# Optimization experiments

Measured on AMD Instinct MI355X. Metric: run time of the kernel, lower is better.

## Reference

```python
import jax, jax.numpy as jnp
import numpy as np

D = 384      # n_embed_dims
H = 6        # n_heads
HS = D // H  # head_size = 64
T = 256      # block_size
B = 256
EPS = 1e-5


def setup_inputs() -> dict:
    key = jax.random.key(0)
    ks = jax.random.split(key, 12)
    s_in = 1.0 / np.sqrt(D)
    s_ff = 1.0 / np.sqrt(4 * D)
    return {
        "x": jax.random.normal(ks[0], (B, T, D), jnp.float32),
        # per-head QKV weights, stacked [H, D, HS] (Linear bias=False)
        "wq": jax.random.normal(ks[1], (H, D, HS), jnp.float32) * s_in,
        "wk": jax.random.normal(ks[2], (H, D, HS), jnp.float32) * s_in,
        "wv": jax.random.normal(ks[3], (H, D, HS), jnp.float32) * s_in,
        "w_proj": jax.random.normal(ks[4], (D, D), jnp.float32) * s_in,
        "b_proj": jax.random.normal(ks[5], (D,), jnp.float32) * s_in,
        "w1": jax.random.normal(ks[6], (D, 4 * D), jnp.float32) * s_in,
        "b1": jax.random.normal(ks[7], (4 * D,), jnp.float32) * s_in,
        "w2": jax.random.normal(ks[8], (4 * D, D), jnp.float32) * s_ff,
        "b2": jax.random.normal(ks[9], (D,), jnp.float32) * s_ff,
        "g1": jnp.ones((D,), jnp.float32),
        "be1": jnp.zeros((D,), jnp.float32),
        "g2": jnp.ones((D,), jnp.float32),
        "be2": jnp.zeros((D,), jnp.float32),
    }


def _layernorm(x, g, b):
    mu = jnp.mean(x, axis=-1, keepdims=True)
    var = jnp.mean(jnp.square(x - mu), axis=-1, keepdims=True)
    return (x - mu) * jax.lax.rsqrt(var + EPS) * g + b


def _attention(x, wq, wk, wv, w_proj, b_proj):
    # faithful quirk: scale = 1/sqrt(C) with C = full embed dim (384)
    scale = 1.0 / jnp.sqrt(jnp.asarray(D, x.dtype))
    q = jnp.einsum("btd,hde->bhte", x, wq)  # [B,H,T,HS]
    k = jnp.einsum("btd,hde->bhte", x, wk)
    v = jnp.einsum("btd,hde->bhte", x, wv)
    w = jnp.einsum("bhte,bhse->bhts", q, k) * scale  # [B,H,T,T], no mask
    w = jax.nn.softmax(w, axis=-1)
    out = jnp.einsum("bhts,bhse->bhte", w, v)  # [B,H,T,HS]
    # concat heads along feature dim (head order matches torch cat)
    out = out.transpose(0, 2, 1, 3).reshape(x.shape[0], x.shape[1], D)
    return out @ w_proj + b_proj


def reference(x, wq, wk, wv, w_proj, b_proj, w1, b1, w2, b2, g1, be1, g2, be2):
    x = x + _attention(_layernorm(x, g1, be1), wq, wk, wv, w_proj, b_proj)
    h = _layernorm(x, g2, be2)
    h = jax.nn.relu(h @ w1 + b1) @ w2 + b2  # dropout = eval-mode identity
    return x + h
```

## Files before the change

kernel.cpp:

```cpp
#include <hip/hip_runtime.h>
#include <stdint.h>

#define NTOK 65536
#define DE 384
#define QSTR 1280

typedef __bf16 bf16x8 __attribute__((ext_vector_type(8)));
typedef float  f32x4 __attribute__((ext_vector_type(4)));
typedef unsigned short u16x8 __attribute__((ext_vector_type(8)));

__device__ __forceinline__ unsigned short f2bf(float f) {
  union { float fl; unsigned u; } a; a.fl = f;
  unsigned r = a.u + 0x7fffu + ((a.u >> 16) & 1u);
  return (unsigned short)(r >> 16);
}
__device__ __forceinline__ float b2f(unsigned short s) {
  union { unsigned u; float f; } v; v.u = (unsigned)s << 16; return v.f;
}

__device__ __forceinline__ void gll16(const void* g, void* l) {
  __builtin_amdgcn_global_load_lds((const __attribute__((address_space(1))) void*)g,
                                   (__attribute__((address_space(3))) void*)l, 16, 0, 0);
}

__device__ __forceinline__ bf16x8 ds128(unsigned addr) {
  bf16x8 r;
  asm volatile("ds_read_b128 %0, %1" : "=v"(r) : "v"(addr));
  return r;
}

__global__ void pack_t(unsigned short* __restrict__ dst, const float* __restrict__ src,
                       int R, int C) {
  int t = blockIdx.x * 256 + threadIdx.x;
  if (t >= R * C) return;
  int r = t / C, c = t - r * C;
  dst[(size_t)c * R + r] = f2bf(src[t]);
}

__global__ void qkv_pack(const float* __restrict__ wq, const float* __restrict__ wk,
                         const float* __restrict__ wv, unsigned short* __restrict__ dst) {
  int t = blockIdx.x * 256 + threadIdx.x;
  if (t >= QSTR * 384) return;
  int n = t / 384, k = t - n * 384;
  unsigned short v = 0;
  if (n < 1152) {
    int which = n / 384, r = n - which * 384;
    const float* src = which == 0 ? wq : (which == 1 ? wk : wv);
    int h = r >> 6, e = r & 63;
    v = f2bf(src[h * 24576 + k * 64 + e]);
  }
  dst[t] = v;
}

__global__ __launch_bounds__(256) void ln_kernel(const float* __restrict__ x,
                                                 const float* __restrict__ g,
                                                 const float* __restrict__ be,
                                                 unsigned short* __restrict__ out) {
  int wave = threadIdx.x >> 6, lane = threadIdx.x & 63;
  size_t row = (size_t)blockIdx.x * 4 + wave;
  const float* xr = x + row * DE;
  int c0 = lane * 2;
  float2 v0 = *(const float2*)(xr + c0);
  float2 v1 = *(const float2*)(xr + 128 + c0);
  float2 v2 = *(const float2*)(xr + 256 + c0);
  float s  = v0.x + v0.y + v1.x + v1.y + v2.x + v2.y;
  float ss = v0.x*v0.x + v0.y*v0.y + v1.x*v1.x + v1.y*v1.y + v2.x*v2.x + v2.y*v2.y;
#pragma unroll
  for (int m = 1; m < 64; m <<= 1) { s += __shfl_xor(s, m); ss += __shfl_xor(ss, m); }
  float mu = s * (1.0f / 384.0f);
  float rstd = rsqrtf(ss * (1.0f / 384.0f) - mu * mu + 1e-5f);
  unsigned short* orow = out + row * DE;
  {
    float a0 = (v0.x - mu) * rstd * g[c0] + be[c0];
    float a1 = (v0.y - mu) * rstd * g[c0 + 1] + be[c0 + 1];
    *(unsigned*)(orow + c0) = (unsigned)f2bf(a0) | ((unsigned)f2bf(a1) << 16);
  }
  {
    int c = c0 + 128;
    float a0 = (v1.x - mu) * rstd * g[c] + be[c];
    float a1 = (v1.y - mu) * rstd * g[c + 1] + be[c + 1];
    *(unsigned*)(orow + c) = (unsigned)f2bf(a0) | ((unsigned)f2bf(a1) << 16);
  }
  {
    int c = c0 + 256;
    float a0 = (v2.x - mu) * rstd * g[c] + be[c];
    float a1 = (v2.y - mu) * rstd * g[c + 1] + be[c + 1];
    *(unsigned*)(orow + c) = (unsigned)f2bf(a0) | ((unsigned)f2bf(a1) << 16);
  }
}

template<int EPI, int BM, int BN, int WM, int WN>
__device__ __forceinline__
void gemm_core(const unsigned short* __restrict__ A, const unsigned short* __restrict__ Bt,
               int M, int K, int Nst, int stride, int ntx,
               const float* __restrict__ bias, const float* __restrict__ residf,
               const unsigned short* __restrict__ residb,
               const float* __restrict__ g2, const float* __restrict__ be2,
               float* __restrict__ outf, unsigned short* __restrict__ outb,
               unsigned short* __restrict__ out2) {
  constexpr int T = WM * WN * 64;
  constexpr int MWT = BM / WM, NWT = BN / WN;
  constexpr int MF = MWT / 16, NF = NWT / 16;
  constexpr int MH = MF / 4;
  constexpr int LA = (BM * 128) / (T * 16);
  constexpr int LB = (BN * 128) / (T * 16);
  __shared__ __align__(16) unsigned short As[2][BM * 64];
  __shared__ __align__(16) unsigned short Bs[2][BN * 64];
  __shared__ float red[BM][4][2];
  const int tid = threadIdx.x;
  const int wave = tid >> 6, lane = tid & 63;

  const int nwg = gridDim.x;
  const int cpx = nwg >> 3;
  const int wg = (blockIdx.x & 7) * cpx + (blockIdx.x >> 3);
  const int bx = wg % ntx, by = wg / ntx;
  const int mBase = by * BM, nBase = bx * BN;
  const int wmi = wave / WN, wni = wave % WN;
  const int wm = wmi * MWT, wn = wni * NWT;
  const int fr = lane & 15, fg = lane >> 4;

  const unsigned asb = (unsigned)(uintptr_t)&As[0][0];
  const unsigned bsb = (unsigned)(uintptr_t)&Bs[0][0];

  f32x4 acc[MF][NF];
  const f32x4 z = {0.f, 0.f, 0.f, 0.f};
#pragma unroll
  for (int i = 0; i < MF; ++i)
#pragma unroll
    for (int j = 0; j < NF; ++j) acc[i][j] = z;

  auto stage = [&](int buf, int kt) {
#pragma unroll
    for (int i = 0; i < LA; ++i) {
      int Lb = i * (T * 16) + wave * 1024;
      int L = Lb + lane * 16;
      int row = L >> 7;
      int col = (((L >> 4) & 7) ^ (row & 7)) << 3;
      gll16(A + (size_t)(mBase + row) * K + kt + col, (unsigned short*)As[buf] + (Lb >> 1));
    }
#pragma unroll
    for (int i = 0; i < LB; ++i) {
      int Lb = i * (T * 16) + wave * 1024;
      int L = Lb + lane * 16;
      int row = L >> 7;
      int col = (((L >> 4) & 7) ^ (row & 7)) << 3;
      gll16(Bt + (size_t)(nBase + row) * K + kt + col, (unsigned short*)Bs[buf] + (Lb >> 1));
    }
  };

  const int NK = K >> 6;
  stage(0, 0);
  for (int t = 0; t < NK; ++t) {
    const int cur = t & 1;
    if (t + 1 < NK) {
      stage(cur ^ 1, (t + 1) << 6);
      if constexpr (LA + LB == 8)      asm volatile("s_waitcnt vmcnt(8)" ::: "memory");
      else if constexpr (LA + LB == 7) asm volatile("s_waitcnt vmcnt(7)" ::: "memory");
      else                             asm volatile("s_waitcnt vmcnt(6)" ::: "memory");
    } else {
      asm volatile("s_waitcnt vmcnt(0)" ::: "memory");
    }
    asm volatile("" ::: "memory");
    __builtin_amdgcn_s_barrier();
    asm volatile("" ::: "memory");

    const unsigned ab = asb + (cur ? (unsigned)(BM * 128) : 0u);
    const unsigned bb = bsb + (cur ? (unsigned)(BN * 128) : 0u);
#pragma unroll
    for (int ks = 0; ks < 2; ++ks) {
      bf16x8 bfr[NF];
#pragma unroll
      for (int nb = 0; nb < NF; ++nb) {
        int row = wn + nb * 16 + fr;
        unsigned byte = (unsigned)(row << 7) + ((unsigned)((ks * 4 + fg) ^ (row & 7)) << 4);
        bfr[nb] = ds128(bb + byte);
      }
#pragma unroll
      for (int mh = 0; mh < MH; ++mh) {
        bf16x8 af[4];
#pragma unroll
        for (int mb = 0; mb < 4; ++mb) {
          int row = wm + (mh * 4 + mb) * 16 + fr;
          unsigned byte = (unsigned)(row << 7) + ((unsigned)((ks * 4 + fg) ^ (row & 7)) << 4);
          af[mb] = ds128(ab + byte);
        }
        asm volatile("s_waitcnt lgkmcnt(0)" ::: "memory");
        __builtin_amdgcn_sched_barrier(0);
        __builtin_amdgcn_s_setprio(1);
#pragma unroll
        for (int mb = 0; mb < 4; ++mb)
#pragma unroll
          for (int nb = 0; nb < NF; ++nb)
            acc[mh * 4 + mb][nb] =
                __builtin_amdgcn_mfma_f32_16x16x32_bf16(af[mb], bfr[nb], acc[mh * 4 + mb][nb], 0, 0, 0);
        __builtin_amdgcn_s_setprio(0);
      }
    }
    asm volatile("" ::: "memory");
    __builtin_amdgcn_s_barrier();
    asm volatile("" ::: "memory");
  }

  if (EPI == 1) {
#pragma unroll
    for (int mb = 0; mb < MF; ++mb) {
#pragma unroll
      for (int nb = 0; nb < NF; ++nb) {
        const int gn = nBase + wn + nb * 16 + fr;
#pragma unroll
        for (int i = 0; i < 4; ++i) {
          const int gm = mBase + wm + mb * 16 + (fg << 2) + i;
          size_t idx = (size_t)gm * stride + gn;
          acc[mb][nb][i] = acc[mb][nb][i] + bias[gn] + residf[idx];
        }
      }
    }
#pragma unroll
    for (int mb = 0; mb < MF; ++mb) {
#pragma unroll
      for (int i = 0; i < 4; ++i) {
        float s = 0.f, ss = 0.f;
#pragma unroll
        for (int nb = 0; nb < NF; ++nb) {
          float v = acc[mb][nb][i];
          s += v; ss += v * v;
        }
        s += __shfl_xor(s, 1); ss += __shfl_xor(ss, 1);
        s += __shfl_xor(s, 2); ss += __shfl_xor(ss, 2);
        s += __shfl_xor(s, 4); ss += __shfl_xor(ss, 4);
        s += __shfl_xor(s, 8); ss += __shfl_xor(ss, 8);
        if (fr == 0) {
          int row = wm + mb * 16 + (fg << 2) + i;
          red[row][wni][0] = s;
          red[row][wni][1] = ss;
        }
      }
    }
    __syncthreads();
#pragma unroll
    for (int mb = 0; mb < MF; ++mb) {
#pragma unroll
      for (int i = 0; i < 4; ++i) {
        int row = wm + mb * 16 + (fg << 2) + i;
        float s = red[row][0][0] + red[row][1][0] + red[row][2][0] + red[row][3][0];
        float ss = red[row][0][1] + red[row][1][1] + red[row][2][1] + red[row][3][1];
        float mu = s * (1.0f / 384.0f);
        float rstd = rsqrtf(ss * (1.0f / 384.0f) - mu * mu + 1e-5f);
        const int gm = mBase + row;
#pragma unroll
        for (int nb = 0; nb < NF; ++nb) {
          const int gn = nBase + wn + nb * 16 + fr;
          size_t idx = (size_t)gm * stride + gn;
          float x1v = acc[mb][nb][i];
          outb[idx] = f2bf(x1v);
          out2[idx] = f2bf((x1v - mu) * rstd * g2[gn] + be2[gn]);
        }
      }
    }
    return;
  }

#pragma unroll
  for (int mb = 0; mb < MF; ++mb) {
#pragma unroll
    for (int nb = 0; nb < NF; ++nb) {
      const int gn = nBase + wn + nb * 16 + fr;
      if (gn < Nst) {
#pragma unroll
        for (int i = 0; i < 4; ++i) {
          const int gm = mBase + wm + mb * 16 + (fg << 2) + i;
          float val = acc[mb][nb][i];
          size_t idx = (size_t)gm * stride + gn;
          if (EPI == 0) {
            outb[idx] = f2bf(val);
          } else if (EPI == 2) {
            float r = val + bias[gn];
            outb[idx] = f2bf(r > 0.f ? r : 0.f);
          } else {
            outf[idx] = val + bias[gn] + b2f(residb[idx]);
          }
        }
      }
    }
  }
}

__global__ __launch_bounds__(512, 1)
void gemm_qkv(const unsigned short* __restrict__ A, const unsigned short* __restrict__ Bt,
              int M, int K, int Nst, int stride, int ntx,
              const float* __restrict__ bias, const float* __restrict__ residf,
              const unsigned short* __restrict__ residb, float* __restrict__ outf,
              unsigned short* __restrict__ outb) {
  gemm_core<0, 256, 192, 2, 4>(A, Bt, M, K, Nst, stride, ntx, bias, residf, residb,
                               nullptr, nullptr, outf, outb, nullptr);
}
__global__ __launch_bounds__(512, 1)
void gemm_projln(const unsigned short* __restrict__ A, const unsigned short* __restrict__ Bt,
                 int M, int K, int Nst, int stride, int ntx,
                 const float* __restrict__ bias, const float* __restrict__ residf,
                 const float* __restrict__ g2, const float* __restrict__ be2,
                 unsigned short* __restrict__ outb, unsigned short* __restrict__ out2) {
  gemm_core<1, 128, 384, 2, 4>(A, Bt, M, K, Nst, stride, ntx, bias, residf, nullptr,
                               g2, be2, nullptr, outb, out2);
}
__global__ __launch_bounds__(512, 1)
void gemm_mlp1(const unsigned short* __restrict__ A, const unsigned short* __restrict__ Bt,
               int M, int K, int Nst, int stride, int ntx,
               const float* __restrict__ bias, const float* __restrict__ residf,
               const unsigned short* __restrict__ residb, float* __restrict__ outf,
               unsigned short* __restrict__ outb) {
  gemm_core<2, 256, 256, 2, 4>(A, Bt, M, K, Nst, stride, ntx, bias, residf, residb,
                               nullptr, nullptr, outf, outb, nullptr);
}
__global__ __launch_bounds__(512, 1)
void gemm_mlp2(const unsigned short* __restrict__ A, const unsigned short* __restrict__ Bt,
               int M, int K, int Nst, int stride, int ntx,
               const float* __restrict__ bias, const float* __restrict__ residf,
               const unsigned short* __restrict__ residb, float* __restrict__ outf,
               unsigned short* __restrict__ outb) {
  gemm_core<3, 256, 128, 4, 2>(A, Bt, M, K, Nst, stride, ntx, bias, residf, residb,
                               nullptr, nullptr, outf, outb, nullptr);
}

__global__ __launch_bounds__(256)
void attn_kernel(const unsigned short* __restrict__ qkvn, unsigned short* __restrict__ o) {
  __shared__ unsigned short Vt[64 * 256];
  __shared__ unsigned short Pw[4][64 * 32];
  const int bh = blockIdx.x;
  const int b = bh / 6, h = bh - b * 6;
  const unsigned short* base = qkvn + (size_t)(b * 256) * QSTR;
  const unsigned short* qb = base + h * 64;
  const unsigned short* kbp = base + 384 + h * 64;
  const unsigned short* vbp = base + 768 + h * 64;
  const int wave = threadIdx.x >> 6, lane = threadIdx.x & 63;
  const int fr = lane & 15, fg = lane >> 4;
  const int fk = fg << 3;
  const int qrow0 = wave << 6;
  const float scale = 0.051031036307982884f;
  const f32x4 z = {0.f, 0.f, 0.f, 0.f};

  {
    const int s = threadIdx.x;
    u16x8 v8[8];
#pragma unroll
    for (int j = 0; j < 8; ++j)
      v8[j] = *(const u16x8*)(vbp + (size_t)s * QSTR + j * 8);
#pragma unroll
    for (int e = 0; e < 64; ++e)
      Vt[(e << 8) + (s ^ ((e & 7) << 3))] = v8[e >> 3][e & 7];
  }
  __syncthreads();

  bf16x8 qf[4][2];
#pragma unroll
  for (int rb = 0; rb < 4; ++rb)
#pragma unroll
    for (int ks = 0; ks < 2; ++ks)
      qf[rb][ks] = *(const bf16x8*)(qb + (size_t)(qrow0 + rb * 16 + fr) * QSTR + ks * 32 + fk);

  f32x4 oacc[4][4];
  float psum[4][4];
#pragma unroll
  for (int rb = 0; rb < 4; ++rb)
#pragma unroll
    for (int nb = 0; nb < 4; ++nb) oacc[rb][nb] = z;
#pragma unroll
  for (int rb = 0; rb < 4; ++rb)
#pragma unroll
    for (int i = 0; i < 4; ++i) psum[rb][i] = 0.f;

  for (int kb2 = 0; kb2 < 8; ++kb2) {
#pragma unroll
    for (int c2 = 0; c2 < 2; ++c2) {
      int cb = kb2 * 2 + c2;
      bf16x8 kf0 = *(const bf16x8*)(kbp + (size_t)(cb * 16 + fr) * QSTR + fk);
      bf16x8 kf1 = *(const bf16x8*)(kbp + (size_t)(cb * 16 + fr) * QSTR + 32 + fk);
#pragma unroll
      for (int rb = 0; rb < 4; ++rb) {
        f32x4 s = __builtin_amdgcn_mfma_f32_16x16x32_bf16(qf[rb][0], kf0, z, 0, 0, 0);
        s = __builtin_amdgcn_mfma_f32_16x16x32_bf16(qf[rb][1], kf1, s, 0, 0, 0);
#pragma unroll
        for (int i = 0; i < 4; ++i) {
          float p = __expf(fminf(scale * s[i], 60.f));
          psum[rb][i] += p;
          Pw[wave][(rb * 16 + (fg << 2) + i) * 32 + c2 * 16 + fr] = f2bf(p);
        }
      }
    }
    bf16x8 pa[4], vf[4];
#pragma unroll
    for (int rb = 0; rb < 4; ++rb) pa[rb] = *(const bf16x8*)(&Pw[wave][(rb * 16 + fr) * 32 + fk]);
#pragma unroll
    for (int nb = 0; nb < 4; ++nb) {
      int e = nb * 16 + fr;
      vf[nb] = *(const bf16x8*)(&Vt[(e << 8) + ((kb2 * 32 + fk) ^ ((e & 7) << 3))]);
    }
#pragma unroll
    for (int rb = 0; rb < 4; ++rb)
#pragma unroll
      for (int nb = 0; nb < 4; ++nb)
        oacc[rb][nb] = __builtin_amdgcn_mfma_f32_16x16x32_bf16(pa[rb], vf[nb], oacc[rb][nb], 0, 0, 0);
  }

  float rs[4][4];
#pragma unroll
  for (int rb = 0; rb < 4; ++rb)
#pragma unroll
    for (int i = 0; i < 4; ++i) {
      float v = psum[rb][i];
      v += __shfl_xor(v, 1);
      v += __shfl_xor(v, 2);
      v += __shfl_xor(v, 4);
      v += __shfl_xor(v, 8);
      rs[rb][i] = 1.0f / v;
    }

#pragma unroll
  for (int rb = 0; rb < 4; ++rb)
#pragma unroll
    for (int nb = 0; nb < 4; ++nb)
#pragma unroll
      for (int i = 0; i < 4; ++i) {
        int token = b * 256 + qrow0 + rb * 16 + (fg << 2) + i;
        int gcol = h * 64 + nb * 16 + fr;
        o[(size_t)token * DE + gcol] = f2bf(oacc[rb][nb][i] * rs[rb][i]);
      }
}

extern "C" void kernel_launch(void* const* d_in, const int* in_sizes, int n_in,
                              void* d_out, int out_size, void* d_ws, size_t ws_size,
                              hipStream_t stream) {
  const float* x     = (const float*)d_in[0];
  const float* wq    = (const float*)d_in[1];
  const float* wk    = (const float*)d_in[2];
  const float* wv    = (const float*)d_in[3];
  const float* wproj = (const float*)d_in[4];
  const float* bproj = (const float*)d_in[5];
  const float* w1    = (const float*)d_in[6];
  const float* b1    = (const float*)d_in[7];
  const float* w2    = (const float*)d_in[8];
  const float* b2    = (const float*)d_in[9];
  const float* g1    = (const float*)d_in[10];
  const float* be1   = (const float*)d_in[11];
  const float* g2    = (const float*)d_in[12];
  const float* be2   = (const float*)d_in[13];

  char* ws = (char*)d_ws;
  unsigned short* xln   = (unsigned short*)(ws + 0);
  unsigned short* x1b   = (unsigned short*)(ws + 0);
  unsigned short* qkvn  = (unsigned short*)(ws + 50331648);
  unsigned short* hbuf  = (unsigned short*)(ws + 100663296);
  unsigned short* act   = (unsigned short*)(ws + 150994944);
  unsigned short* attno = (unsigned short*)(ws + 218103808);
  unsigned short* wqkvt = (unsigned short*)(ws + 352321536);
  unsigned short* wprjt = (unsigned short*)(ws + 352321536 + 983040);
  unsigned short* w1t   = (unsigned short*)(ws + 352321536 + 983040 + 294912);
  unsigned short* w2t   = (unsigned short*)(ws + 352321536 + 983040 + 294912 + 1179648);

  qkv_pack<<<(QSTR * 384 + 255) / 256, 256, 0, stream>>>(wq, wk, wv, wqkvt);
  pack_t<<<(147456 + 255) / 256, 256, 0, stream>>>(wprjt, wproj, 384, 384);
  pack_t<<<(589824 + 255) / 256, 256, 0, stream>>>(w1t, w1, 384, 1536);
  pack_t<<<(589824 + 255) / 256, 256, 0, stream>>>(w2t, w2, 1536, 384);

  ln_kernel<<<NTOK / 4, 256, 0, stream>>>(x, g1, be1, xln);

  gemm_qkv<<<6 * 256, 512, 0, stream>>>(xln, wqkvt, NTOK, 384, 1152, 1280, 6,
                                        nullptr, nullptr, nullptr, nullptr, qkvn);

  attn_kernel<<<1536, 256, 0, stream>>>(qkvn, attno);

  gemm_projln<<<512, 512, 0, stream>>>(attno, wprjt, NTOK, 384, 384, 384, 1,
                                       bproj, x, g2, be2, x1b, hbuf);

  gemm_mlp1<<<6 * 256, 512, 0, stream>>>(hbuf, w1t, NTOK, 384, 1536, 1536, 6,
                                         b1, nullptr, nullptr, nullptr, act);

  gemm_mlp2<<<3 * 256, 512, 0, stream>>>(act, w2t, NTOK, 1536, 384, 384, 3,
                                         b2, nullptr, x1b, (float*)d_out, nullptr);
}
```

Measured before the change: 530.0 us.

## Switch GEMM core to 32x32x16 bf16 MFMA tiles

Replaces the 16x16x32 MFMA fragments in the shared GEMM core with 32x32x16 MFMA operating on 16-float accumulators, reworking the LDS fragment addressing, the K-step loop (two k-substeps batched before one wait), and all epilogue row/column mappings including the fused LayerNorm reduction. The larger MFMA shape gives more math per LDS fragment load, reducing LDS read traffic and instruction count. The QKV kernel's wave grid changes from 2x4 to 4x2 so per-wave tiles divide into 32-wide blocks. The risks are higher register pressure from the larger accumulators and a different store pattern in the epilogue.

```diff
diff --git a/kernel.cpp b/kernel.cpp
--- a/kernel.cpp
+++ b/kernel.cpp
@@ -6,7 +6,8 @@
 #define QSTR 1280
 
 typedef __bf16 bf16x8 __attribute__((ext_vector_type(8)));
-typedef float  f32x4 __attribute__((ext_vector_type(4)));
+typedef float  f32x4  __attribute__((ext_vector_type(4)));
+typedef float  f32x16 __attribute__((ext_vector_type(16)));
 typedef unsigned short u16x8 __attribute__((ext_vector_type(8)));
 
 __device__ __forceinline__ unsigned short f2bf(float f) {
@@ -100,13 +101,12 @@
                unsigned short* __restrict__ out2) {
   constexpr int T = WM * WN * 64;
   constexpr int MWT = BM / WM, NWT = BN / WN;
-  constexpr int MF = MWT / 16, NF = NWT / 16;
-  constexpr int MH = MF / 4;
+  constexpr int MT = MWT / 32, NT = NWT / 32;
   constexpr int LA = (BM * 128) / (T * 16);
   constexpr int LB = (BN * 128) / (T * 16);
   __shared__ __align__(16) unsigned short As[2][BM * 64];
   __shared__ __align__(16) unsigned short Bs[2][BN * 64];
-  __shared__ float red[BM][4][2];
+  __shared__ float red[(EPI == 1) ? BM : 1][4][2];
   const int tid = threadIdx.x;
   const int wave = tid >> 6, lane = tid & 63;
 
@@ -117,17 +117,19 @@
   const int mBase = by * BM, nBase = bx * BN;
   const int wmi = wave / WN, wni = wave % WN;
   const int wm = wmi * MWT, wn = wni * NWT;
-  const int fr = lane & 15, fg = lane >> 4;
+  const int cr = lane & 31;
+  const int hg = lane >> 5;
 
   const unsigned asb = (unsigned)(uintptr_t)&As[0][0];
   const unsigned bsb = (unsigned)(uintptr_t)&Bs[0][0];
 
-  f32x4 acc[MF][NF];
-  const f32x4 z = {0.f, 0.f, 0.f, 0.f};
-#pragma unroll
-  for (int i = 0; i < MF; ++i)
-#pragma unroll
-    for (int j = 0; j < NF; ++j) acc[i][j] = z;
+  f32x16 acc[MT][NT];
+#pragma unroll
+  for (int i = 0; i < MT; ++i)
+#pragma unroll
+    for (int j = 0; j < NT; ++j)
+#pragma unroll
+      for (int r = 0; r < 16; ++r) acc[i][j][r] = 0.f;
 
   auto stage = [&](int buf, int kt) {
 #pragma unroll
@@ -167,34 +169,36 @@
     const unsigned ab = asb + (cur ? (unsigned)(BM * 128) : 0u);
     const unsigned bb = bsb + (cur ? (unsigned)(BN * 128) : 0u);
 #pragma unroll
-    for (int ks = 0; ks < 2; ++ks) {
-      bf16x8 bfr[NF];
-#pragma unroll
-      for (int nb = 0; nb < NF; ++nb) {
-        int row = wn + nb * 16 + fr;
-        unsigned byte = (unsigned)(row << 7) + ((unsigned)((ks * 4 + fg) ^ (row & 7)) << 4);
-        bfr[nb] = ds128(bb + byte);
-      }
-#pragma unroll
-      for (int mh = 0; mh < MH; ++mh) {
-        bf16x8 af[4];
-#pragma unroll
-        for (int mb = 0; mb < 4; ++mb) {
-          int row = wm + (mh * 4 + mb) * 16 + fr;
-          unsigned byte = (unsigned)(row << 7) + ((unsigned)((ks * 4 + fg) ^ (row & 7)) << 4);
-          af[mb] = ds128(ab + byte);
-        }
-        asm volatile("s_waitcnt lgkmcnt(0)" ::: "memory");
-        __builtin_amdgcn_sched_barrier(0);
-        __builtin_amdgcn_s_setprio(1);
-#pragma unroll
-        for (int mb = 0; mb < 4; ++mb)
-#pragma unroll
-          for (int nb = 0; nb < NF; ++nb)
-            acc[mh * 4 + mb][nb] =
-                __builtin_amdgcn_mfma_f32_16x16x32_bf16(af[mb], bfr[nb], acc[mh * 4 + mb][nb], 0, 0, 0);
-        __builtin_amdgcn_s_setprio(0);
-      }
+    for (int k2 = 0; k2 < 2; ++k2) {
+      bf16x8 bfr[2][NT], af[2][MT];
+#pragma unroll
+      for (int kk = 0; kk < 2; ++kk) {
+        const int ks = k2 * 2 + kk;
+#pragma unroll
+        for (int nt = 0; nt < NT; ++nt) {
+          int row = wn + nt * 32 + cr;
+          unsigned byte = (unsigned)(row << 7) + ((unsigned)((ks * 2 + hg) ^ (row & 7)) << 4);
+          bfr[kk][nt] = ds128(bb + byte);
+        }
+#pragma unroll
+        for (int mt = 0; mt < MT; ++mt) {
+          int row = wm + mt * 32 + cr;
+          unsigned byte = (unsigned)(row << 7) + ((unsigned)((ks * 2 + hg) ^ (row & 7)) << 4);
+          af[kk][mt] = ds128(ab + byte);
+        }
+      }
+      asm volatile("s_waitcnt lgkmcnt(0)" ::: "memory");
+      __builtin_amdgcn_sched_barrier(0);
+      __builtin_amdgcn_s_setprio(1);
+#pragma unroll
+      for (int kk = 0; kk < 2; ++kk)
+#pragma unroll
+        for (int mt = 0; mt < MT; ++mt)
+#pragma unroll
+          for (int nt = 0; nt < NT; ++nt)
+            acc[mt][nt] = __builtin_amdgcn_mfma_f32_32x32x16_bf16(af[kk][mt], bfr[kk][nt],
+                                                                  acc[mt][nt], 0, 0, 0);
+      __builtin_amdgcn_s_setprio(0);
     }
     asm volatile("" ::: "memory");
     __builtin_amdgcn_s_barrier();
@@ -203,34 +207,35 @@
 
   if (EPI == 1) {
 #pragma unroll
-    for (int mb = 0; mb < MF; ++mb) {
-#pragma unroll
-      for (int nb = 0; nb < NF; ++nb) {
-        const int gn = nBase + wn + nb * 16 + fr;
-#pragma unroll
-        for (int i = 0; i < 4; ++i) {
-          const int gm = mBase + wm + mb * 16 + (fg << 2) + i;
+    for (int mt = 0; mt < MT; ++mt) {
+#pragma unroll
+      for (int nt = 0; nt < NT; ++nt) {
+        const int gn = nBase + wn + nt * 32 + cr;
+#pragma unroll
+        for (int r = 0; r < 16; ++r) {
+          const int gm = mBase + wm + mt * 32 + (r & 3) + ((r >> 2) << 3) + (hg << 2);
           size_t idx = (size_t)gm * stride + gn;
-          acc[mb][nb][i] = acc[mb][nb][i] + bias[gn] + residf[idx];
-        }
-      }
-    }
-#pragma unroll
-    for (int mb = 0; mb < MF; ++mb) {
-#pragma unroll
-      for (int i = 0; i < 4; ++i) {
+          acc[mt][nt][r] = acc[mt][nt][r] + bias[gn] + residf[idx];
+        }
+      }
+    }
+#pragma unroll
+    for (int mt = 0; mt < MT; ++mt) {
+#pragma unroll
+      for (int r = 0; r < 16; ++r) {
         float s = 0.f, ss = 0.f;
 #pragma unroll
-        for (int nb = 0; nb < NF; ++nb) {
-          float v = acc[mb][nb][i];
+        for (int nt = 0; nt < NT; ++nt) {
+          float v = acc[mt][nt][r];
           s += v; ss += v * v;
         }
-        s += __shfl_xor(s, 1); ss += __shfl_xor(ss, 1);
-        s += __shfl_xor(s, 2); ss += __shfl_xor(ss, 2);
-        s += __shfl_xor(s, 4); ss += __shfl_xor(ss, 4);
-        s += __shfl_xor(s, 8); ss += __shfl_xor(ss, 8);
-        if (fr == 0) {
-          int row = wm + mb * 16 + (fg << 2) + i;
+        s += __shfl_xor(s, 1);  ss += __shfl_xor(ss, 1);
+        s += __shfl_xor(s, 2);  ss += __shfl_xor(ss, 2);
+        s += __shfl_xor(s, 4);  ss += __shfl_xor(ss, 4);
+        s += __shfl_xor(s, 8);  ss += __shfl_xor(ss, 8);
+        s += __shfl_xor(s, 16); ss += __shfl_xor(ss, 16);
+        if (cr == 0) {
+          int row = wm + mt * 32 + (r & 3) + ((r >> 2) << 3) + (hg << 2);
           red[row][wni][0] = s;
           red[row][wni][1] = ss;
         }
@@ -238,20 +243,20 @@
     }
     __syncthreads();
 #pragma unroll
-    for (int mb = 0; mb < MF; ++mb) {
-#pragma unroll
-      for (int i = 0; i < 4; ++i) {
-        int row = wm + mb * 16 + (fg << 2) + i;
+    for (int mt = 0; mt < MT; ++mt) {
+#pragma unroll
+      for (int r = 0; r < 16; ++r) {
+        int row = wm + mt * 32 + (r & 3) + ((r >> 2) << 3) + (hg << 2);
         float s = red[row][0][0] + red[row][1][0] + red[row][2][0] + red[row][3][0];
         float ss = red[row][0][1] + red[row][1][1] + red[row][2][1] + red[row][3][1];
         float mu = s * (1.0f / 384.0f);
         float rstd = rsqrtf(ss * (1.0f / 384.0f) - mu * mu + 1e-5f);
         const int gm = mBase + row;
 #pragma unroll
-        for (int nb = 0; nb < NF; ++nb) {
-          const int gn = nBase + wn + nb * 16 + fr;
+        for (int nt = 0; nt < NT; ++nt) {
+          const int gn = nBase + wn + nt * 32 + cr;
           size_t idx = (size_t)gm * stride + gn;
-          float x1v = acc[mb][nb][i];
+          float x1v = acc[mt][nt][r];
           outb[idx] = f2bf(x1v);
           out2[idx] = f2bf((x1v - mu) * rstd * g2[gn] + be2[gn]);
         }
@@ -261,21 +266,21 @@
   }
 
 #pragma unroll
-  for (int mb = 0; mb < MF; ++mb) {
-#pragma unroll
-    for (int nb = 0; nb < NF; ++nb) {
-      const int gn = nBase + wn + nb * 16 + fr;
+  for (int mt = 0; mt < MT; ++mt) {
+#pragma unroll
+    for (int nt = 0; nt < NT; ++nt) {
+      const int gn = nBase + wn + nt * 32 + cr;
       if (gn < Nst) {
 #pragma unroll
-        for (int i = 0; i < 4; ++i) {
-          const int gm = mBase + wm + mb * 16 + (fg << 2) + i;
-          float val = acc[mb][nb][i];
+        for (int r = 0; r < 16; ++r) {
+          const int gm = mBase + wm + mt * 32 + (r & 3) + ((r >> 2) << 3) + (hg << 2);
+          float val = acc[mt][nt][r];
           size_t idx = (size_t)gm * stride + gn;
           if (EPI == 0) {
             outb[idx] = f2bf(val);
           } else if (EPI == 2) {
-            float r = val + bias[gn];
-            outb[idx] = f2bf(r > 0.f ? r : 0.f);
+            float rr = val + bias[gn];
+            outb[idx] = f2bf(rr > 0.f ? rr : 0.f);
           } else {
             outf[idx] = val + bias[gn] + b2f(residb[idx]);
           }
@@ -291,7 +296,7 @@
               const float* __restrict__ bias, const float* __restrict__ residf,
               const unsigned short* __restrict__ residb, float* __restrict__ outf,
               unsigned short* __restrict__ outb) {
-  gemm_core<0, 256, 192, 2, 4>(A, Bt, M, K, Nst, stride, ntx, bias, residf, residb,
+  gemm_core<0, 256, 192, 4, 2>(A, Bt, M, K, Nst, stride, ntx, bias, residf, residb,
                                nullptr, nullptr, outf, outb, nullptr);
 }
 __global__ __launch_bounds__(512, 1)
```

New measurement: 517.9 us. 2.3% less time.
